# Performance work log

Hardware: AMD Instinct MI355X
Metric: run time of the kernel (lower is better)

Reference implementation:

```python
import jax, jax.numpy as jnp
import numpy as np

B, C, H, W = 8, 8, 512, 512

# one-pixel shifts with zero padding (equivalent to the bmm with shift matrices)
def shift_right(x):  # out[..., c] = x[..., c-1]
    return jnp.pad(x, ((0, 0), (0, 0), (1, 0)))[:, :, :-1]
def shift_left(x):   # out[..., c] = x[..., c+1]
    return jnp.pad(x, ((0, 0), (0, 0), (0, 1)))[:, :, 1:]
def shift_up(x):     # out[r] = x[r+1]
    return jnp.pad(x, ((0, 0), (0, 1), (0, 0)))[:, 1:, :]
def shift_down(x):   # out[r] = x[r-1]
    return jnp.pad(x, ((0, 0), (1, 0), (0, 0)))[:, :-1, :]

def bilater_voting(c):
    # c: [B, 8, H, W] probabilities
    right        = shift_right(c[:, 4])
    left         = shift_left(c[:, 3])
    left_bottom  = shift_left(shift_down(c[:, 5]))
    right_above  = shift_right(shift_up(c[:, 2]))
    left_above   = shift_left(shift_up(c[:, 0]))
    bottom       = shift_down(c[:, 6])
    up           = shift_up(c[:, 1])
    right_bottom = shift_right(shift_down(c[:, 7]))
    a1 = c[:, 3] * right
    a2 = c[:, 4] * left
    a3 = c[:, 1] * bottom
    a4 = c[:, 6] * up
    a5 = c[:, 2] * left_bottom
    a6 = c[:, 5] * right_above
    a7 = c[:, 0] * right_bottom
    a8 = c[:, 7] * left_above
    vote_out = jnp.stack([a7, a3, a5, a1, a2, a6, a4, a8], axis=1)
    glo_map = jnp.mean(vote_out, axis=1)
    return glo_map, vote_out

def bce(p, t):
    # matches torch F.binary_cross_entropy (mean reduction, log clamped at -100)
    logp = jnp.clip(jnp.log(p), -100.0, None)
    log1mp = jnp.clip(jnp.log(1.0 - p), -100.0, None)
    return -jnp.mean(t * logp + (1.0 - t) * log1mp)

def setup_inputs() -> dict:
    key = jax.random.key(0)
    k1, k2, k3, k4 = jax.random.split(key, 4)
    atts = jax.random.normal(k1, (B, C, H, W), dtype=jnp.float32)
    dets = jax.random.normal(k2, (B, C, H, W), dtype=jnp.float32)
    target = jax.random.randint(k3, (B, 1, H, W), 0, 2).astype(jnp.float32)
    con_target = jax.random.randint(k4, (B, C, H, W), 0, 2).astype(jnp.float32)
    return {"atts": atts, "dets": dets, "target": target, "con_target": con_target}

def reference(atts, dets, target, con_target):
    # edge mask from connectivity GT: pixels with 0 < sum < 8
    sum_conn = jnp.sum(con_target, axis=1)  # [B, H, W]
    edge_conn = jnp.where((sum_conn < 8.0) & (sum_conn > 0.0), 1.0, 0.0)

    atts_p = jax.nn.sigmoid(atts)
    dets_p = jax.nn.sigmoid(dets)

    glo_map1, vote_out1 = bilater_voting(atts_p)
    glo_map2, vote_out2 = bilater_voting(dets_p)

    # edge/decouple loss on dets branch
    pred_mask_min = 1.0 - jnp.min(vote_out2, axis=1)
    pred_mask_min = pred_mask_min * edge_conn
    decouple_map = glo_map2 * (1.0 - edge_conn) + pred_mask_min
    de_loss2 = bce(decouple_map[:, None], target)

    bce_loss1 = bce(glo_map1[:, None], target)
    bicon_loss1 = bce(vote_out1, con_target)
    conn_loss1 = bce(atts_p, con_target)
    bicon_loss2 = bce(vote_out2, con_target)
    conn_loss2 = bce(dets_p, con_target)

    loss = (0.2 * bicon_loss1 + 0.8 * conn_loss1 + bce_loss1
            + 0.2 * bicon_loss2 + 0.8 * conn_loss2 + de_loss2)
    return loss
```

## Files before the change

### kernel.cpp

```cpp
#include <hip/hip_runtime.h>

#define BB 8
#define CC 8
#define HH 512
#define WW 512
#define HWSZ (HH * WW)

typedef float v4 __attribute__((ext_vector_type(4)));

#define LOG2_CLAMP -144.26950409f

__device__ __forceinline__ v4 uload4(const float* __restrict__ p) {
    v4 r;
    __builtin_memcpy(&r, p, sizeof(v4));
    return r;
}
__device__ __forceinline__ v4 aload4(const float* __restrict__ p) {
    return *(const v4* __restrict__)p;
}

__device__ __forceinline__ v4 sig4(v4 x) {
    v4 r;
#pragma unroll
    for (int i = 0; i < 4; ++i)
        r[i] = __builtin_amdgcn_rcpf(1.0f + __expf(-x[i]));
    return r;
}

__device__ __forceinline__ v4 vsel(v4 t, v4 x, v4 y) {
    v4 r;
#pragma unroll
    for (int i = 0; i < 4; ++i) r[i] = (t[i] > 0.5f) ? x[i] : y[i];
    return r;
}

template <bool NEED_MIN>
__device__ __forceinline__ void eval_branch(
    const v4* __restrict__ cr, const v4* __restrict__ nr,
    const v4* __restrict__ cv, const v4* __restrict__ mk,
    v4& glo, v4& vmin, float& Lbic, float& Lcon)
{
    v4 pb0 = {1.f, 1.f, 1.f, 1.f}, pb1 = {1.f, 1.f, 1.f, 1.f};
    v4 pc  = {1.f, 1.f, 1.f, 1.f};
    v4 vsum = {0.f, 0.f, 0.f, 0.f};
    if (NEED_MIN) vmin = {1e30f, 1e30f, 1e30f, 1e30f};
    v4 one = {1.f, 1.f, 1.f, 1.f};

#pragma unroll
    for (int k = 0; k < 8; ++k) {
        v4 s = sig4(cr[k]);
        v4 n = sig4(nr[k]) * mk[k];
        v4 v = s * n;
        vsum += v;
        if (NEED_MIN) vmin = __builtin_elementwise_min(vmin, v);
        v4 t  = cv[k];
        v4 av = vsel(t, v, one - v);
        v4 as = vsel(t, s, one - s);
        if (k < 4) pb0 *= av; else pb1 *= av;
        pc *= as;
    }
    glo = vsum * 0.125f;

    float lb = 0.f, lc = 0.f;
#pragma unroll
    for (int i = 0; i < 4; ++i) {
        lb += fmaxf(__log2f(pb0[i]), LOG2_CLAMP) + fmaxf(__log2f(pb1[i]), LOG2_CLAMP);
        lc += fmaxf(__log2f(pc[i]), LOG2_CLAMP);
    }
    Lbic = lb;
    Lcon = lc;
}

__global__ __launch_bounds__(256, 2) void bicon_loss_kernel(
    const float* __restrict__ atts, const float* __restrict__ dets,
    const float* __restrict__ target, const float* __restrict__ con,
    float* __restrict__ out)
{
    const int idx = blockIdx.x * 256 + threadIdx.x;
    const int w0  = (idx & 127) << 2;
    const int row = idx >> 7;
    const int h   = row & (HH - 1);
    const int b   = row >> 9;

    const int hm = (h > 0) ? h - 1 : 0;
    const int hp = (h < HH - 1) ? h + 1 : HH - 1;
    const float mh0 = (h > 0) ? 1.0f : 0.0f;
    const float mh1 = (h < HH - 1) ? 1.0f : 0.0f;
    const v4 mwL = {(w0 == 0) ? 0.0f : 1.0f, 1.f, 1.f, 1.f};
    const v4 mwR = {1.f, 1.f, 1.f, (w0 == WW - 4) ? 0.0f : 1.0f};

    const int offC = h * WW + w0;
    const int offU = hm * WW + w0;
    const int offD = hp * WW + w0;

    const float* __restrict__ ab = atts + b * CC * HWSZ;
    const float* __restrict__ db = dets + b * CC * HWSZ;
    const float* __restrict__ cb = con  + b * CC * HWSZ;

    v4 ac[8], an[8], dc[8], dn[8], cv[8], t4;
#pragma unroll
    for (int c = 0; c < 8; ++c) ac[c] = aload4(ab + c * HWSZ + offC);
    an[0] = uload4(ab + 7 * HWSZ + offU - 1);
    an[1] = aload4(ab + 6 * HWSZ + offU);
    an[2] = uload4(ab + 5 * HWSZ + offU + 1);
    an[3] = uload4(ab + 4 * HWSZ + offC - 1);
    an[4] = uload4(ab + 3 * HWSZ + offC + 1);
    an[5] = uload4(ab + 2 * HWSZ + offD - 1);
    an[6] = aload4(ab + 1 * HWSZ + offD);
    an[7] = uload4(ab + 0 * HWSZ + offD + 1);
#pragma unroll
    for (int c = 0; c < 8; ++c) dc[c] = aload4(db + c * HWSZ + offC);
    dn[0] = uload4(db + 7 * HWSZ + offU - 1);
    dn[1] = aload4(db + 6 * HWSZ + offU);
    dn[2] = uload4(db + 5 * HWSZ + offU + 1);
    dn[3] = uload4(db + 4 * HWSZ + offC - 1);
    dn[4] = uload4(db + 3 * HWSZ + offC + 1);
    dn[5] = uload4(db + 2 * HWSZ + offD - 1);
    dn[6] = aload4(db + 1 * HWSZ + offD);
    dn[7] = uload4(db + 0 * HWSZ + offD + 1);
#pragma unroll
    for (int c = 0; c < 8; ++c) cv[c] = aload4(cb + c * HWSZ + offC);
    t4 = aload4(target + b * HWSZ + offC);

    v4 mk[8];
    mk[0] = mwL * mh0;
    mk[1] = {mh0, mh0, mh0, mh0};
    mk[2] = mwR * mh0;
    mk[3] = mwL;
    mk[4] = mwR;
    mk[5] = mwL * mh1;
    mk[6] = {mh1, mh1, mh1, mh1};
    mk[7] = mwR * mh1;

    v4 csum = {0.f, 0.f, 0.f, 0.f};
#pragma unroll
    for (int c = 0; c < 8; ++c) csum += cv[c];
    v4 edge;
#pragma unroll
    for (int i = 0; i < 4; ++i)
        edge[i] = (csum[i] < 8.0f && csum[i] > 0.0f) ? 1.0f : 0.0f;

    v4 glo1, glo2, vmin1, vmin2;
    float Lb1, Lc1, Lb2, Lc2;
    eval_branch<false>(ac, an, cv, mk, glo1, vmin1, Lb1, Lc1);
    eval_branch<true >(dc, dn, cv, mk, glo2, vmin2, Lb2, Lc2);

    float Lp = 0.f;
#pragma unroll
    for (int i = 0; i < 4; ++i) {
        float dec = (edge[i] > 0.5f) ? (1.0f - vmin2[i]) : glo2[i];
        float a  = (t4[i] > 0.5f) ? glo1[i] : 1.0f - glo1[i];
        float bs = (t4[i] > 0.5f) ? dec     : 1.0f - dec;
        Lp += fmaxf(__log2f(a * bs), LOG2_CLAMP);
    }

    const float wbic = 0.2f / (float)(BB * CC * HWSZ);
    const float wcon = 0.8f / (float)(BB * CC * HWSZ);
    const float wpix = 1.0f / (float)(BB * HWSZ);
    const float ln2  = 0.69314718056f;

    float local = -(wbic * (Lb1 + Lb2) + wcon * (Lc1 + Lc2) + wpix * Lp) * ln2;

#pragma unroll
    for (int off = 32; off > 0; off >>= 1)
        local += __shfl_down(local, off, 64);

    __shared__ float wsum[4];
    const int lane = threadIdx.x & 63;
    const int wid  = threadIdx.x >> 6;
    if (lane == 0) wsum[wid] = local;
    __syncthreads();
    if (threadIdx.x == 0) {
        float s = wsum[0] + wsum[1] + wsum[2] + wsum[3];
        atomicAdd(out, s);
    }
}

extern "C" void kernel_launch(void* const* d_in, const int* in_sizes, int n_in,
                              void* d_out, int out_size, void* d_ws, size_t ws_size,
                              hipStream_t stream) {
    const float* atts   = (const float*)d_in[0];
    const float* dets   = (const float*)d_in[1];
    const float* target = (const float*)d_in[2];
    const float* con    = (const float*)d_in[3];
    float* out = (float*)d_out;

    hipMemsetAsync(out, 0, sizeof(float), stream);

    const int ngroups = BB * HH * WW / 4;
    bicon_loss_kernel<<<ngroups / 256, 256, 0, stream>>>(atts, dets, target, con, out);
}
```

Before: 200.8 us.

## Reuse center sigmoids via lane shuffles instead of reloading shifted neighbors

Horizontal neighbor values are now built from already-loaded, already-sigmoided center vectors via cross-lane shuffles, with edge lanes fetching a single scalar. Only three up-row and three down-row channels are loaded per branch, and all loads are now aligned. This cuts redundant sigmoid evaluations and unaligned global loads, at the cost of extra shuffles and divergent scalar edge loads. The occupancy hint of 2 in the launch bounds is dropped.

```diff
diff --git a/kernel.cpp b/kernel.cpp
--- a/kernel.cpp
+++ b/kernel.cpp
@@ -5,57 +5,82 @@
 #define HH 512
 #define WW 512
 #define HWSZ (HH * WW)
+#define CHW (CC * HWSZ)
 
 typedef float v4 __attribute__((ext_vector_type(4)));
 
 #define LOG2_CLAMP -144.26950409f
 
-__device__ __forceinline__ v4 uload4(const float* __restrict__ p) {
-    v4 r;
-    __builtin_memcpy(&r, p, sizeof(v4));
-    return r;
+__device__ __forceinline__ float sigf(float x) {
+    return __builtin_amdgcn_rcpf(1.0f + __expf(-x));
 }
 __device__ __forceinline__ v4 aload4(const float* __restrict__ p) {
     return *(const v4* __restrict__)p;
 }
-
 __device__ __forceinline__ v4 sig4(v4 x) {
     v4 r;
 #pragma unroll
-    for (int i = 0; i < 4; ++i)
-        r[i] = __builtin_amdgcn_rcpf(1.0f + __expf(-x[i]));
-    return r;
-}
-
-__device__ __forceinline__ v4 vsel(v4 t, v4 x, v4 y) {
+    for (int i = 0; i < 4; ++i) r[i] = sigf(x[i]);
+    return r;
+}
+__device__ __forceinline__ v4 vsel(v4 t, v4 a, v4 b) {
     v4 r;
 #pragma unroll
-    for (int i = 0; i < 4; ++i) r[i] = (t[i] > 0.5f) ? x[i] : y[i];
+    for (int i = 0; i < 4; ++i) r[i] = (t[i] > 0.5f) ? a[i] : b[i];
+    return r;
+}
+
+__device__ __forceinline__ v4 mk_left(v4 s, float e, int lane) {
+    float y = __shfl_up(s[3], 1, 64);
+    y = (lane == 0) ? e : y;
+    v4 r = {y, s[0], s[1], s[2]};
+    return r;
+}
+__device__ __forceinline__ v4 mk_right(v4 s, float e, int lane) {
+    float x = __shfl_down(s[0], 1, 64);
+    x = (lane == 63) ? e : x;
+    v4 r = {s[1], s[2], s[3], x};
     return r;
 }
 
 template <bool NEED_MIN>
 __device__ __forceinline__ void eval_branch(
-    const v4* __restrict__ cr, const v4* __restrict__ nr,
-    const v4* __restrict__ cv, const v4* __restrict__ mk,
+    const float* __restrict__ base, int oC, int oU, int oD,
+    float mh0, float mh1, v4 mwL, v4 mwR,
+    const v4* __restrict__ cv, const float* eL, const float* eR, int lane,
     v4& glo, v4& vmin, float& Lbic, float& Lcon)
 {
-    v4 pb0 = {1.f, 1.f, 1.f, 1.f}, pb1 = {1.f, 1.f, 1.f, 1.f};
-    v4 pc  = {1.f, 1.f, 1.f, 1.f};
-    v4 vsum = {0.f, 0.f, 0.f, 0.f};
+    v4 s[8];
+#pragma unroll
+    for (int c = 0; c < 8; ++c) s[c] = sig4(aload4(base + c * HWSZ + oC));
+    v4 s5m = sig4(aload4(base + 5 * HWSZ + oU));
+    v4 s6m = sig4(aload4(base + 6 * HWSZ + oU));
+    v4 s7m = sig4(aload4(base + 7 * HWSZ + oU));
+    v4 s0p = sig4(aload4(base + 0 * HWSZ + oD));
+    v4 s1p = sig4(aload4(base + 1 * HWSZ + oD));
+    v4 s2p = sig4(aload4(base + 2 * HWSZ + oD));
+
+    v4 n[8];
+    n[0] = mk_left (s7m,  eL[1], lane) * (mh0 * mwL);
+    n[1] = s6m * mh0;
+    n[2] = mk_right(s5m,  eR[1], lane) * (mh0 * mwR);
+    n[3] = mk_left (s[4], eL[0], lane) * mwL;
+    n[4] = mk_right(s[3], eR[0], lane) * mwR;
+    n[5] = mk_left (s2p,  eL[2], lane) * (mh1 * mwL);
+    n[6] = s1p * mh1;
+    n[7] = mk_right(s0p,  eR[2], lane) * (mh1 * mwR);
+
+    v4 one = {1.f, 1.f, 1.f, 1.f};
+    v4 pb0 = one, pb1 = one, pc = one, vsum = {0.f, 0.f, 0.f, 0.f};
     if (NEED_MIN) vmin = {1e30f, 1e30f, 1e30f, 1e30f};
-    v4 one = {1.f, 1.f, 1.f, 1.f};
-
 #pragma unroll
     for (int k = 0; k < 8; ++k) {
-        v4 s = sig4(cr[k]);
-        v4 n = sig4(nr[k]) * mk[k];
-        v4 v = s * n;
+        v4 v = s[k] * n[k];
         vsum += v;
         if (NEED_MIN) vmin = __builtin_elementwise_min(vmin, v);
         v4 t  = cv[k];
         v4 av = vsel(t, v, one - v);
-        v4 as = vsel(t, s, one - s);
+        v4 as = vsel(t, s[k], one - s[k]);
         if (k < 4) pb0 *= av; else pb1 *= av;
         pc *= as;
     }
@@ -71,7 +96,7 @@
     Lcon = lc;
 }
 
-__global__ __launch_bounds__(256, 2) void bicon_loss_kernel(
+__global__ __launch_bounds__(256) void bicon_loss_kernel(
     const float* __restrict__ atts, const float* __restrict__ dets,
     const float* __restrict__ target, const float* __restrict__ con,
     float* __restrict__ out)
@@ -81,6 +106,7 @@
     const int row = idx >> 7;
     const int h   = row & (HH - 1);
     const int b   = row >> 9;
+    const int lane = threadIdx.x & 63;
 
     const int hm = (h > 0) ? h - 1 : 0;
     const int hp = (h < HH - 1) ? h + 1 : HH - 1;
@@ -89,68 +115,61 @@
     const v4 mwL = {(w0 == 0) ? 0.0f : 1.0f, 1.f, 1.f, 1.f};
     const v4 mwR = {1.f, 1.f, 1.f, (w0 == WW - 4) ? 0.0f : 1.0f};
 
-    const int offC = h * WW + w0;
-    const int offU = hm * WW + w0;
-    const int offD = hp * WW + w0;
-
-    const float* __restrict__ ab = atts + b * CC * HWSZ;
-    const float* __restrict__ db = dets + b * CC * HWSZ;
-    const float* __restrict__ cb = con  + b * CC * HWSZ;
-
-    v4 ac[8], an[8], dc[8], dn[8], cv[8], t4;
-#pragma unroll
-    for (int c = 0; c < 8; ++c) ac[c] = aload4(ab + c * HWSZ + offC);
-    an[0] = uload4(ab + 7 * HWSZ + offU - 1);
-    an[1] = aload4(ab + 6 * HWSZ + offU);
-    an[2] = uload4(ab + 5 * HWSZ + offU + 1);
-    an[3] = uload4(ab + 4 * HWSZ + offC - 1);
-    an[4] = uload4(ab + 3 * HWSZ + offC + 1);
-    an[5] = uload4(ab + 2 * HWSZ + offD - 1);
-    an[6] = aload4(ab + 1 * HWSZ + offD);
-    an[7] = uload4(ab + 0 * HWSZ + offD + 1);
-#pragma unroll
-    for (int c = 0; c < 8; ++c) dc[c] = aload4(db + c * HWSZ + offC);
-    dn[0] = uload4(db + 7 * HWSZ + offU - 1);
-    dn[1] = aload4(db + 6 * HWSZ + offU);
-    dn[2] = uload4(db + 5 * HWSZ + offU + 1);
-    dn[3] = uload4(db + 4 * HWSZ + offC - 1);
-    dn[4] = uload4(db + 3 * HWSZ + offC + 1);
-    dn[5] = uload4(db + 2 * HWSZ + offD - 1);
-    dn[6] = aload4(db + 1 * HWSZ + offD);
-    dn[7] = uload4(db + 0 * HWSZ + offD + 1);
-#pragma unroll
-    for (int c = 0; c < 8; ++c) cv[c] = aload4(cb + c * HWSZ + offC);
-    t4 = aload4(target + b * HWSZ + offC);
-
-    v4 mk[8];
-    mk[0] = mwL * mh0;
-    mk[1] = {mh0, mh0, mh0, mh0};
-    mk[2] = mwR * mh0;
-    mk[3] = mwL;
-    mk[4] = mwR;
-    mk[5] = mwL * mh1;
-    mk[6] = {mh1, mh1, mh1, mh1};
-    mk[7] = mwR * mh1;
-
+    const int oC = h * WW + w0;
+    const int oU = hm * WW + w0;
+    const int oD = hp * WW + w0;
+
+    const float* __restrict__ ab = atts + b * CHW;
+    const float* __restrict__ db = dets + b * CHW;
+    const float* __restrict__ cb = con  + b * CHW;
+
+    v4 cv[8];
     v4 csum = {0.f, 0.f, 0.f, 0.f};
 #pragma unroll
-    for (int c = 0; c < 8; ++c) csum += cv[c];
+    for (int c = 0; c < 8; ++c) {
+        cv[c] = aload4(cb + c * HWSZ + oC);
+        csum += cv[c];
+    }
     v4 edge;
 #pragma unroll
     for (int i = 0; i < 4; ++i)
         edge[i] = (csum[i] < 8.0f && csum[i] > 0.0f) ? 1.0f : 0.0f;
-
-    v4 glo1, glo2, vmin1, vmin2;
+    const v4 t4 = aload4(target + b * HWSZ + oC);
+
+    float eLA[3] = {0.f, 0.f, 0.f}, eRA[3] = {0.f, 0.f, 0.f};
+    float eLD[3] = {0.f, 0.f, 0.f}, eRD[3] = {0.f, 0.f, 0.f};
+    if (lane == 0) {
+        const int wl = (w0 > 0) ? w0 - 1 : 0;
+        eLA[0] = sigf(ab[4 * HWSZ + h  * WW + wl]);
+        eLA[1] = sigf(ab[7 * HWSZ + hm * WW + wl]);
+        eLA[2] = sigf(ab[2 * HWSZ + hp * WW + wl]);
+        eLD[0] = sigf(db[4 * HWSZ + h  * WW + wl]);
+        eLD[1] = sigf(db[7 * HWSZ + hm * WW + wl]);
+        eLD[2] = sigf(db[2 * HWSZ + hp * WW + wl]);
+    }
+    if (lane == 63) {
+        const int w2 = (w0 + 4 < WW) ? w0 + 4 : WW - 1;
+        eRA[0] = sigf(ab[3 * HWSZ + h  * WW + w2]);
+        eRA[1] = sigf(ab[5 * HWSZ + hm * WW + w2]);
+        eRA[2] = sigf(ab[0 * HWSZ + hp * WW + w2]);
+        eRD[0] = sigf(db[3 * HWSZ + h  * WW + w2]);
+        eRD[1] = sigf(db[5 * HWSZ + hm * WW + w2]);
+        eRD[2] = sigf(db[0 * HWSZ + hp * WW + w2]);
+    }
+
+    v4 glo1, glo2, vmin2, dum;
     float Lb1, Lc1, Lb2, Lc2;
-    eval_branch<false>(ac, an, cv, mk, glo1, vmin1, Lb1, Lc1);
-    eval_branch<true >(dc, dn, cv, mk, glo2, vmin2, Lb2, Lc2);
+    eval_branch<false>(ab, oC, oU, oD, mh0, mh1, mwL, mwR, cv, eLA, eRA, lane,
+                       glo1, dum, Lb1, Lc1);
+    eval_branch<true >(db, oC, oU, oD, mh0, mh1, mwL, mwR, cv, eLD, eRD, lane,
+                       glo2, vmin2, Lb2, Lc2);
 
     float Lp = 0.f;
 #pragma unroll
     for (int i = 0; i < 4; ++i) {
         float dec = (edge[i] > 0.5f) ? (1.0f - vmin2[i]) : glo2[i];
-        float a  = (t4[i] > 0.5f) ? glo1[i] : 1.0f - glo1[i];
-        float bs = (t4[i] > 0.5f) ? dec     : 1.0f - dec;
+        float a   = (t4[i] > 0.5f) ? glo1[i] : 1.0f - glo1[i];
+        float bs  = (t4[i] > 0.5f) ? dec     : 1.0f - dec;
         Lp += fmaxf(__log2f(a * bs), LOG2_CLAMP);
     }
 
@@ -166,8 +185,7 @@
         local += __shfl_down(local, off, 64);
 
     __shared__ float wsum[4];
-    const int lane = threadIdx.x & 63;
-    const int wid  = threadIdx.x >> 6;
+    const int wid = threadIdx.x >> 6;
     if (lane == 0) wsum[wid] = local;
     __syncthreads();
     if (threadIdx.x == 0) {
```

Result: no change. 203.8 us (+1.5%).
